# Kernel tuning notes

Measured on AMD Instinct MI355X. Metric: run time of the kernel, lower is better.

Reference implementation:

```python
import jax, jax.numpy as jnp
import numpy as np

N_FEATURES = 256
TOPK = 32
WINDOW = 128
EMBED = 128
BATCH = 64
ALPHA = 0.2  # LeakyReLU negative slope


def setup_inputs() -> dict:
    key = jax.random.key(0)
    ks = jax.random.split(key, 8)
    x_n = jax.random.normal(ks[0], (BATCH, N_FEATURES, WINDOW), jnp.float32)
    x_e = jax.random.normal(ks[1], (N_FEATURES, TOPK), jnp.float32)
    edge_indices = jax.random.randint(ks[2], (2, N_FEATURES * TOPK), 0, N_FEATURES, dtype=jnp.int32)
    all_embeddings = jax.random.normal(ks[3], (N_FEATURES, EMBED), jnp.float32)
    # lin_n: Linear(window_size, embed_dim)
    W_n = jax.random.normal(ks[4], (WINDOW, EMBED), jnp.float32) * (1.0 / np.sqrt(WINDOW))
    b_n = jax.random.normal(ks[5], (EMBED,), jnp.float32) * 0.01
    # attention vector a: [2*embed_dim, 1], xavier-like scale
    a = jax.random.normal(ks[6], (2 * EMBED, 1), jnp.float32) * (1.414 / np.sqrt(2 * EMBED))
    bias_n = jax.random.normal(ks[7], (N_FEATURES, TOPK), jnp.float32) * 0.02
    return {"x_n": x_n, "x_e": x_e, "edge_indices": edge_indices,
            "all_embeddings": all_embeddings, "W_n": W_n, "b_n": b_n,
            "a": a, "bias_n": bias_n}


def reference(x_n, x_e, edge_indices, all_embeddings, W_n, b_n, a, bias_n):
    B, NF, _ = x_n.shape
    K, E = TOPK, EMBED
    lrelu = lambda t: jax.nn.leaky_relu(t, negative_slope=ALPHA)

    # Wx_n = lin_n(x_n): [B, NF, E]
    Wx_n = jnp.einsum('bnw,we->bne', x_n, W_n) + b_n

    nbr = edge_indices[0].reshape(NF, K)  # neighbor ids per node

    # _make_node_attention_input (faithful, including the cat-then-view mixing):
    # repeat_interleave(K, dim=1) -> [B, NF, K, E]
    rep = jnp.broadcast_to(Wx_n[:, :, None, :], (B, NF, K, E))
    alt = Wx_n[:, nbr]  # gather: [B, NF, K, E]
    # cat on dim=2 -> [B, NF, 2K, E]; view -> [B, NF, K, 2E]
    a_input_n = jnp.concatenate([rep, alt], axis=2).reshape(B, NF, K, 2 * E)

    # e_n = leakyrelu(a_input_n @ a).squeeze(3): [B, NF, K]
    e_n = lrelu(jnp.einsum('bnkd,d->bnk', a_input_n, a[:, 0]))
    e_n = e_n + jnp.nan_to_num(bias_n)

    # softmax over topk neighbors; dropout is a no-op in eval mode
    attention_n = jax.nn.softmax(e_n, axis=2)

    # weighted aggregate of gathered neighbor features
    h_n = lrelu(attention_n[..., None] * alt)  # [B, NF, K, E]
    return h_n
```

## Files before the change

kernel.cpp:

```cpp
#include <hip/hip_runtime.h>

#define NFEAT 256
#define TK    32
#define WIN   128
#define EMB   128
#define NBATCH 64
#define ALPHA 0.2f
#define MROWS (NBATCH * NFEAT)

__device__ __forceinline__ float lrelu(float x) { return x > 0.f ? x : ALPHA * x; }

__global__ __launch_bounds__(256) void gemm_wx(
    const float* __restrict__ x,
    const float* __restrict__ W,
    const float* __restrict__ bn,
    const float* __restrict__ avec,
    float* __restrict__ wx,
    float* __restrict__ s1, float* __restrict__ s2) {
  __shared__ float xT[WIN][36];
  int t = threadIdx.x;
  int rows0 = blockIdx.x * 32;

  {
    int r = t >> 3, jc = t & 7;
    const float4* src = (const float4*)(x + (long)(rows0 + r) * WIN + jc * 16);
#pragma unroll
    for (int u = 0; u < 4; ++u) {
      float4 v = src[u];
      int c = jc * 16 + u * 4;
      xT[c + 0][r] = v.x; xT[c + 1][r] = v.y; xT[c + 2][r] = v.z; xT[c + 3][r] = v.w;
    }
  }
  __syncthreads();

  int g = t >> 5, ct = t & 31;
  int r0 = g * 4;
  int c0 = ct * 4;

  float acc[4][4];
#pragma unroll
  for (int i = 0; i < 4; ++i)
#pragma unroll
    for (int j = 0; j < 4; ++j) acc[i][j] = 0.f;

#pragma unroll 4
  for (int k = 0; k < WIN; ++k) {
    float4 xv = *(const float4*)&xT[k][r0];
    float4 wv = *(const float4*)(W + k * EMB + c0);
    acc[0][0] += xv.x * wv.x; acc[0][1] += xv.x * wv.y; acc[0][2] += xv.x * wv.z; acc[0][3] += xv.x * wv.w;
    acc[1][0] += xv.y * wv.x; acc[1][1] += xv.y * wv.y; acc[1][2] += xv.y * wv.z; acc[1][3] += xv.y * wv.w;
    acc[2][0] += xv.z * wv.x; acc[2][1] += xv.z * wv.y; acc[2][2] += xv.z * wv.z; acc[2][3] += xv.z * wv.w;
    acc[3][0] += xv.w * wv.x; acc[3][1] += xv.w * wv.y; acc[3][2] += xv.w * wv.z; acc[3][3] += xv.w * wv.w;
  }

  float4 bv = *(const float4*)(bn + c0);
#pragma unroll
  for (int i = 0; i < 4; ++i) {
    acc[i][0] += bv.x; acc[i][1] += bv.y; acc[i][2] += bv.z; acc[i][3] += bv.w;
  }

#pragma unroll
  for (int i = 0; i < 4; ++i) {
    float4 o = make_float4(acc[i][0], acc[i][1], acc[i][2], acc[i][3]);
    *(float4*)(wx + (long)(rows0 + r0 + i) * EMB + c0) = o;
  }

  float4 a1 = *(const float4*)(avec + c0);
  float4 a2 = *(const float4*)(avec + EMB + c0);
  float p1[4], p2[4];
#pragma unroll
  for (int i = 0; i < 4; ++i) {
    p1[i] = acc[i][0] * a1.x + acc[i][1] * a1.y + acc[i][2] * a1.z + acc[i][3] * a1.w;
    p2[i] = acc[i][0] * a2.x + acc[i][1] * a2.y + acc[i][2] * a2.z + acc[i][3] * a2.w;
  }
#pragma unroll
  for (int i = 0; i < 4; ++i) {
#pragma unroll
    for (int m = 1; m < 32; m <<= 1) {
      p1[i] += __shfl_xor(p1[i], m, 64);
      p2[i] += __shfl_xor(p2[i], m, 64);
    }
  }
  if (ct == 0) {
#pragma unroll
    for (int i = 0; i < 4; ++i) {
      s1[rows0 + r0 + i] = p1[i];
      s2[rows0 + r0 + i] = p2[i];
    }
  }
}

__global__ __launch_bounds__(256) void attn_out(
    const int* __restrict__ edge,
    const float* __restrict__ biasn,
    const float* __restrict__ wx,
    const float* __restrict__ s1, const float* __restrict__ s2,
    float* __restrict__ out) {
  __shared__ float att[TK];
  __shared__ int nbrS[TK];
  int bidx = blockIdx.x;
  int b = bidx >> 8, n = bidx & 255;
  int tid = threadIdx.x;

  if (tid < TK) {
    int k = tid;
    nbrS[k] = edge[n * TK + k];
    float v;
    if (k < 16) {
      v = s1[b * NFEAT + n] + s2[b * NFEAT + n];
    } else {
      int j0 = 2 * k - 32;
      int r0 = edge[n * TK + j0];
      int r1 = edge[n * TK + j0 + 1];
      v = s1[b * NFEAT + r0] + s2[b * NFEAT + r1];
    }
    v = lrelu(v);
    float bb = biasn[n * TK + k];
    if (bb != bb) bb = 0.f;
    v += bb;
    float mx = v;
#pragma unroll
    for (int m = 1; m < 32; m <<= 1) mx = fmaxf(mx, __shfl_xor(mx, m, 64));
    float ex = __expf(v - mx);
    float sum = ex;
#pragma unroll
    for (int m = 1; m < 32; m <<= 1) sum += __shfl_xor(sum, m, 64);
    att[k] = ex / sum;
  }
  __syncthreads();

  int kq = tid >> 5;
  int c  = (tid & 31) * 4;
#pragma unroll
  for (int p = 0; p < 4; ++p) {
    int k = kq + p * 8;
    long row = (long)b * NFEAT + nbrS[k];
    float ak = att[k];
    float4 v = *(const float4*)(wx + row * EMB + c);
    float4 o = make_float4(lrelu(ak * v.x), lrelu(ak * v.y),
                           lrelu(ak * v.z), lrelu(ak * v.w));
    *(float4*)(out + ((long)bidx * TK + k) * EMB + c) = o;
  }
}

extern "C" void kernel_launch(void* const* d_in, const int* in_sizes, int n_in,
                              void* d_out, int out_size, void* d_ws, size_t ws_size,
                              hipStream_t stream) {
  const float* x_n    = (const float*)d_in[0];
  const int*   edge   = (const int*)d_in[2];
  const float* W_n    = (const float*)d_in[4];
  const float* b_n    = (const float*)d_in[5];
  const float* a_v    = (const float*)d_in[6];
  const float* bias_n = (const float*)d_in[7];
  float* out = (float*)d_out;

  char* ws = (char*)d_ws;
  float* wx = (float*)ws;
  float* s1 = (float*)(ws + (8 << 20));
  float* s2 = (float*)(ws + (8 << 20) + (64 << 10));

  gemm_wx<<<MROWS / 32, 256, 0, stream>>>(x_n, W_n, b_n, a_v, wx, s1, s2);
  attn_out<<<NBATCH * NFEAT, 256, 0, stream>>>(edge, bias_n, wx, s1, s2, out);
}
```

Before: 304.2 us.

## Split attention into coefficient kernel and grid-stride streaming output kernel

Replaces the per-(batch,node) attention/output kernel with two kernels. The first computes softmax coefficients for 8 nodes per block using all 256 threads, and packs each attention weight with its gathered row index into an int2 buffer. The second is a persistent grid-stride kernel that streams the 268MB output, reading the packed record and gathering wx rows. This removes the idle threads and the syncthreads in the old per-block softmax phase, at the cost of one more launch and an extra small workspace round trip.

```diff
diff --git a/kernel.cpp b/kernel.cpp
--- a/kernel.cpp
+++ b/kernel.cpp
@@ -90,56 +90,59 @@
   }
 }
 
-__global__ __launch_bounds__(256) void attn_out(
+__global__ __launch_bounds__(256) void attn_coef(
     const int* __restrict__ edge,
     const float* __restrict__ biasn,
+    const float* __restrict__ s1, const float* __restrict__ s2,
+    int2* __restrict__ pk) {
+  int tid = threadIdx.x;
+  int k  = tid & 31;
+  int nl = tid >> 5;
+  int bidx = blockIdx.x * 8 + nl;
+  int b = bidx >> 8, n = bidx & 255;
+
+  int nbr = edge[n * TK + k];
+  float v;
+  if (k < 16) {
+    v = s1[b * NFEAT + n] + s2[b * NFEAT + n];
+  } else {
+    int j0 = 2 * k - 32;
+    int r0 = edge[n * TK + j0];
+    int r1 = edge[n * TK + j0 + 1];
+    v = s1[b * NFEAT + r0] + s2[b * NFEAT + r1];
+  }
+  v = lrelu(v);
+  float bb = biasn[n * TK + k];
+  if (bb != bb) bb = 0.f;
+  v += bb;
+  float mx = v;
+#pragma unroll
+  for (int m = 1; m < 32; m <<= 1) mx = fmaxf(mx, __shfl_xor(mx, m, 64));
+  float ex = __expf(v - mx);
+  float sum = ex;
+#pragma unroll
+  for (int m = 1; m < 32; m <<= 1) sum += __shfl_xor(sum, m, 64);
+  float att = ex / sum;
+
+  int2 rec;
+  rec.x = __float_as_int(att);
+  rec.y = b * NFEAT + nbr;
+  pk[bidx * TK + k] = rec;
+}
+
+__global__ __launch_bounds__(256) void stream_out(
+    const int2* __restrict__ pk,
     const float* __restrict__ wx,
-    const float* __restrict__ s1, const float* __restrict__ s2,
-    float* __restrict__ out) {
-  __shared__ float att[TK];
-  __shared__ int nbrS[TK];
-  int bidx = blockIdx.x;
-  int b = bidx >> 8, n = bidx & 255;
-  int tid = threadIdx.x;
-
-  if (tid < TK) {
-    int k = tid;
-    nbrS[k] = edge[n * TK + k];
-    float v;
-    if (k < 16) {
-      v = s1[b * NFEAT + n] + s2[b * NFEAT + n];
-    } else {
-      int j0 = 2 * k - 32;
-      int r0 = edge[n * TK + j0];
-      int r1 = edge[n * TK + j0 + 1];
-      v = s1[b * NFEAT + r0] + s2[b * NFEAT + r1];
-    }
-    v = lrelu(v);
-    float bb = biasn[n * TK + k];
-    if (bb != bb) bb = 0.f;
-    v += bb;
-    float mx = v;
-#pragma unroll
-    for (int m = 1; m < 32; m <<= 1) mx = fmaxf(mx, __shfl_xor(mx, m, 64));
-    float ex = __expf(v - mx);
-    float sum = ex;
-#pragma unroll
-    for (int m = 1; m < 32; m <<= 1) sum += __shfl_xor(sum, m, 64);
-    att[k] = ex / sum;
-  }
-  __syncthreads();
-
-  int kq = tid >> 5;
-  int c  = (tid & 31) * 4;
-#pragma unroll
-  for (int p = 0; p < 4; ++p) {
-    int k = kq + p * 8;
-    long row = (long)b * NFEAT + nbrS[k];
-    float ak = att[k];
-    float4 v = *(const float4*)(wx + row * EMB + c);
+    float4* __restrict__ out) {
+  const unsigned total = (unsigned)MROWS * TK * (EMB / 4);
+  unsigned gsz = gridDim.x * blockDim.x;
+  for (unsigned i = blockIdx.x * blockDim.x + threadIdx.x; i < total; i += gsz) {
+    int2 p = pk[i >> 5];
+    float ak = __int_as_float(p.x);
+    float4 v = *(const float4*)(wx + (long)p.y * EMB + (i & 31) * 4);
     float4 o = make_float4(lrelu(ak * v.x), lrelu(ak * v.y),
                            lrelu(ak * v.z), lrelu(ak * v.w));
-    *(float4*)(out + ((long)bidx * TK + k) * EMB + c) = o;
+    out[i] = o;
   }
 }
 
@@ -158,7 +161,9 @@
   float* wx = (float*)ws;
   float* s1 = (float*)(ws + (8 << 20));
   float* s2 = (float*)(ws + (8 << 20) + (64 << 10));
+  int2*  pk = (int2*)(ws + (8 << 20) + (128 << 10));
 
   gemm_wx<<<MROWS / 32, 256, 0, stream>>>(x_n, W_n, b_n, a_v, wx, s1, s2);
-  attn_out<<<NBATCH * NFEAT, 256, 0, stream>>>(edge, bias_n, wx, s1, s2, out);
+  attn_coef<<<MROWS / 8, 256, 0, stream>>>(edge, bias_n, s1, s2, pk);
+  stream_out<<<2048, 256, 0, stream>>>(pk, wx, (float4*)out);
 }
```

Measured after the change: 308.0 us. No clear change (+1.2%).
